# Optimization experiments

Measured on AMD Instinct MI355X. Metric: run time of the kernel, lower is better.

Reference implementation:

```python
import jax, jax.numpy as jnp
import numpy as np


def positional_encoding(n_tokens, d_model, dtype=jnp.float32):
    # standard sinusoidal PE: pe[pos, 2i] = sin(pos / 10000^(2i/d)), pe[pos, 2i+1] = cos(...)
    pos = jnp.arange(n_tokens, dtype=dtype)[:, None]            # [n, 1]
    i = jnp.arange(0, d_model, 2, dtype=dtype)[None, :]         # [1, d/2]
    angle = pos / jnp.power(jnp.asarray(10000.0, dtype), i / d_model)
    pe = jnp.zeros((n_tokens, d_model), dtype)
    pe = pe.at[:, 0::2].set(jnp.sin(angle))
    pe = pe.at[:, 1::2].set(jnp.cos(angle))
    return pe


def layer_norm(x, gamma, beta, eps=1e-5):
    mu = jnp.mean(x, axis=-1, keepdims=True)
    var = jnp.var(x, axis=-1, keepdims=True)
    return (x - mu) * jax.lax.rsqrt(var + eps) * gamma + beta


def setup_inputs() -> dict:
    key = jax.random.key(0)
    ks = jax.random.split(key, 4)
    b, n, d = 4, 1024, 1024
    dh = 1024  # dim_hidden_linear
    s = 1.0 / np.sqrt(d)
    return {
        "token_embedding": jax.random.normal(ks[0], (b, n, d), jnp.float32),
        "ln_gamma": jnp.ones((d,), jnp.float32),
        "ln_beta": jnp.zeros((d,), jnp.float32),
        "Wq": jax.random.normal(ks[1], (d, dh), jnp.float32) * s,
        "bq": jnp.zeros((dh,), jnp.float32),
        "Wk": jax.random.normal(ks[2], (d, dh), jnp.float32) * s,
        "bk": jnp.zeros((dh,), jnp.float32),
        "Wv": jax.random.normal(ks[3], (d, dh), jnp.float32) * s,
        "bv": jnp.zeros((dh,), jnp.float32),
        "num_heads": 16,
    }


def reference(token_embedding, ln_gamma, ln_beta, Wq, bq, Wk, bk, Wv, bv, num_heads):
    b, n, d = token_embedding.shape
    pe = positional_encoding(n, d)                      # [n, d]
    x = token_embedding + pe[None, :, :]                # broadcast over batch
    x = layer_norm(x, ln_gamma, ln_beta)
    q = x @ Wq + bq                                     # [b, n, dh]
    k = x @ Wk + bk
    v = x @ Wv + bv
    dh = q.shape[-1]
    hd = dh // num_heads                                # per-head dim
    q = q.reshape(b, n, num_heads, hd)
    k = k.reshape(b, n, num_heads, hd)
    v = v.reshape(b, n, num_heads, hd)
    scale = 1.0 / jnp.sqrt(jnp.asarray(hd, q.dtype))
    scores = jnp.einsum("bqhd,bkhd->bhqk", q, k) * scale  # [b, h, n, n]
    attn = jax.nn.softmax(scores, axis=-1)
    out = jnp.einsum("bhqk,bkhd->bqhd", attn, v)          # [b, n, h, hd]
    return out.reshape(b, n, dh)
```

## Files before the change

### kernel.cpp

```cpp
#include <hip/hip_runtime.h>
#include <hip/hip_bf16.h>
#include <math.h>

typedef __attribute__((ext_vector_type(8))) short bf16x8;
typedef __attribute__((ext_vector_type(4))) short bf16x4;
typedef __attribute__((ext_vector_type(4))) float f32x4;

static __device__ __forceinline__ void gld16(const void* g, void* l) {
    __builtin_amdgcn_global_load_lds(
        (const __attribute__((address_space(1))) unsigned int*)g,
        (__attribute__((address_space(3))) unsigned int*)l, 16, 0, 0);
}

static __device__ __forceinline__ short f2bf_s(float f) {
    __hip_bfloat16 h = __float2bfloat16(f);
    short s;
    __builtin_memcpy(&s, &h, 2);
    return s;
}

__global__ __launch_bounds__(256) void peln_wt_kernel(
    const float* __restrict__ emb,
    const float* __restrict__ gamma,
    const float* __restrict__ beta,
    const float* __restrict__ Wq,
    const float* __restrict__ Wk,
    const float* __restrict__ Wv,
    __hip_bfloat16* __restrict__ x,
    __hip_bfloat16* __restrict__ Wt)
{
    const int tid = threadIdx.x;
    if (blockIdx.x < 4096) {
        const int row = blockIdx.x;
        const int t   = row & 1023;
        float4 e = ((const float4*)(emb + (size_t)row * 1024))[tid];
        float v[4] = {e.x, e.y, e.z, e.w};
        float s = 0.f, ss = 0.f;
        #pragma unroll
        for (int kk = 0; kk < 4; ++kk) {
            int c = tid * 4 + kk;
            float ang = (float)t * exp2f(-13.287712379549449f * (float)(c >> 1) * (1.0f / 512.0f));
            float pe  = (c & 1) ? __cosf(ang) : __sinf(ang);
            v[kk] += pe;
            s  += v[kk];
            ss += v[kk] * v[kk];
        }
        #pragma unroll
        for (int off = 1; off < 64; off <<= 1) {
            s  += __shfl_xor(s, off);
            ss += __shfl_xor(ss, off);
        }
        __shared__ float red_s[4], red_ss[4];
        int wave = tid >> 6, lane = tid & 63;
        if (lane == 0) { red_s[wave] = s; red_ss[wave] = ss; }
        __syncthreads();
        float S  = red_s[0] + red_s[1] + red_s[2] + red_s[3];
        float SS = red_ss[0] + red_ss[1] + red_ss[2] + red_ss[3];
        float mu   = S * (1.0f / 1024.0f);
        float var  = SS * (1.0f / 1024.0f) - mu * mu;
        float rstd = rsqrtf(var + 1e-5f);
        #pragma unroll
        for (int kk = 0; kk < 4; ++kk) {
            int c = tid * 4 + kk;
            float y = (v[kk] - mu) * rstd * gamma[c] + beta[c];
            x[(size_t)row * 1024 + c] = __float2bfloat16(y);
        }
    } else {
        __shared__ __hip_bfloat16 tile[32][33];
        int wid = blockIdx.x - 4096;
        int zz  = wid >> 10;
        int rem = wid & 1023;
        int bx = rem & 31, by = rem >> 5;
        int tx = tid & 31, ty = tid >> 5;
        const float* src = (zz == 0) ? Wq : (zz == 1) ? Wk : Wv;
        __hip_bfloat16* dst = Wt + (size_t)zz * 1024 * 1024;
        int x0 = bx * 32, y0 = by * 32;
        #pragma unroll
        for (int kk = 0; kk < 4; ++kk)
            tile[ty + 8 * kk][tx] =
                __float2bfloat16(src[(size_t)(y0 + ty + 8 * kk) * 1024 + x0 + tx]);
        __syncthreads();
        #pragma unroll
        for (int kk = 0; kk < 4; ++kk)
            dst[(size_t)(x0 + ty + 8 * kk) * 1024 + y0 + tx] = tile[tx][ty + 8 * kk];
    }
}

__global__ __launch_bounds__(256) void qkv_gemm(
    const __hip_bfloat16* __restrict__ X,
    const __hip_bfloat16* __restrict__ Wt,
    const float* __restrict__ bq,
    const float* __restrict__ bk,
    const float* __restrict__ bv,
    __hip_bfloat16* __restrict__ qkv,
    __hip_bfloat16* __restrict__ vt)
{
    union SMem {
        struct { __hip_bfloat16 A[128 * 64]; __hip_bfloat16 B[128 * 64]; } s;
        __hip_bfloat16 C[128 * 132];
    };
    __shared__ __align__(16) SMem sm;

    const int id   = blockIdx.x;
    const int xcd  = id & 7;
    const int rest = id >> 3;
    const int j    = rest % 3;
    const int mblk = rest / 3;
    const int m0   = mblk * 128;
    const int n0   = (xcd * 3 + j) * 128;
    const int t    = n0 >> 10;
    const int nn0  = n0 & 1023;
    const __hip_bfloat16* W = Wt + (size_t)t * 1024 * 1024;

    const int tid  = threadIdx.x;
    const int wave = tid >> 6, lane = tid & 63;
    const int wm = wave & 1, wn = wave >> 1;
    const int lm = lane & 15, quad = lane >> 4;

    const int srow = lane >> 3;
    const int skc  = ((lane & 7) ^ srow) * 8;
    const int rbase = wave * 32;
    const __hip_bfloat16* gA = X + (size_t)(m0 + rbase + srow) * 1024 + skc;
    const __hip_bfloat16* gB = W + (size_t)(nn0 + rbase + srow) * 1024 + skc;
    __hip_bfloat16* lA = sm.s.A + rbase * 64;
    __hip_bfloat16* lB = sm.s.B + rbase * 64;

    f32x4 acc[4][4];
    #pragma unroll
    for (int i = 0; i < 4; ++i)
        #pragma unroll
        for (int jj = 0; jj < 4; ++jj)
            acc[i][jj] = (f32x4){0.f, 0.f, 0.f, 0.f};

    #pragma unroll
    for (int n = 0; n < 4; ++n) {
        gld16(gA + (size_t)n * 8 * 1024, lA + n * 8 * 64);
        gld16(gB + (size_t)n * 8 * 1024, lB + n * 8 * 64);
    }

    for (int k0 = 0; k0 < 1024; k0 += 64) {
        __syncthreads();

        bf16x8 a[2][4], b[2][4];
        #pragma unroll
        for (int ks = 0; ks < 2; ++ks) {
            #pragma unroll
            for (int i = 0; i < 4; ++i) {
                int row = wm * 64 + i * 16 + lm;
                a[ks][i] = *(const bf16x8*)(sm.s.A + (size_t)row * 64
                                            + (((ks * 4 + quad) ^ (lm & 7)) * 8));
            }
            #pragma unroll
            for (int jj = 0; jj < 4; ++jj) {
                int row = wn * 64 + jj * 16 + lm;
                b[ks][jj] = *(const bf16x8*)(sm.s.B + (size_t)row * 64
                                             + (((ks * 4 + quad) ^ (lm & 7)) * 8));
            }
        }
        __syncthreads();

        if (k0 + 64 < 1024) {
            #pragma unroll
            for (int n = 0; n < 4; ++n) {
                gld16(gA + (size_t)n * 8 * 1024 + k0 + 64, lA + n * 8 * 64);
                gld16(gB + (size_t)n * 8 * 1024 + k0 + 64, lB + n * 8 * 64);
            }
        }

        #pragma unroll
        for (int ks = 0; ks < 2; ++ks)
            #pragma unroll
            for (int i = 0; i < 4; ++i)
                #pragma unroll
                for (int jj = 0; jj < 4; ++jj)
                    acc[i][jj] = __builtin_amdgcn_mfma_f32_16x16x32_bf16(a[ks][i], b[ks][jj], acc[i][jj], 0, 0, 0);
    }

    const float* bias = (t == 0) ? bq : (t == 1) ? bk : bv;
    if (t < 2) {
        #pragma unroll
        for (int jj = 0; jj < 4; ++jj) {
            int col = wn * 64 + jj * 16 + lm;
            float bb = bias[nn0 + col];
            #pragma unroll
            for (int i = 0; i < 4; ++i)
                #pragma unroll
                for (int r = 0; r < 4; ++r) {
                    int row = wm * 64 + i * 16 + quad * 4 + r;
                    sm.C[(size_t)row * 132 + col] = __float2bfloat16(acc[i][jj][r] + bb);
                }
        }
        __syncthreads();
        __hip_bfloat16* out = qkv + (size_t)t * 4096 * 1024;
        #pragma unroll
        for (int c = 0; c < 8; ++c) {
            int g = tid + 256 * c;
            int row = g >> 4;
            int colc = (g & 15) * 8;
            bf16x8 vch = *(const bf16x8*)&sm.C[(size_t)row * 132 + colc];
            *(bf16x8*)(out + (size_t)(m0 + row) * 1024 + nn0 + colc) = vch;
        }
    } else {
        #pragma unroll
        for (int jj = 0; jj < 4; ++jj) {
            int col = wn * 64 + jj * 16 + lm;
            float bb = bias[nn0 + col];
            #pragma unroll
            for (int i = 0; i < 4; ++i)
                #pragma unroll
                for (int r = 0; r < 4; ++r) {
                    int row = wm * 64 + i * 16 + quad * 4 + r;
                    sm.C[(size_t)col * 132 + row] = __float2bfloat16(acc[i][jj][r] + bb);
                }
        }
        __syncthreads();
        const int bbase = (m0 >> 10) * 16 + (nn0 >> 6);
        const int mloc  = m0 & 1023;
        #pragma unroll
        for (int c = 0; c < 8; ++c) {
            int g = tid + 256 * c;
            int col = g >> 4;
            int rch = (g & 15) * 8;
            bf16x8 vch = *(const bf16x8*)&sm.C[(size_t)col * 132 + rch];
            int bh = bbase + (col >> 6);
            int d  = col & 63;
            *(bf16x8*)(vt + ((size_t)bh * 64 + d) * 1024 + mloc + rch) = vch;
        }
    }
}

__global__ __launch_bounds__(256, 2) void attn_kernel(
    const __hip_bfloat16* __restrict__ q,
    const __hip_bfloat16* __restrict__ k,
    const __hip_bfloat16* __restrict__ vt,
    float* __restrict__ out)
{
    __shared__ __align__(16) __hip_bfloat16 Kbuf[128 * 64];
    __shared__ __align__(16) __hip_bfloat16 Vbuf[2][64 * 64];
    __shared__ short ldsPT[4][32][72];
    const int id   = blockIdx.x;
    const int bh   = (id & 7) * 8 + ((id >> 3) & 7);
    const int qblk = id >> 6;
    const int b = bh >> 4, h = bh & 15;
    const int wave = threadIdx.x >> 6, lane = threadIdx.x & 63;
    const int lm = lane & 15, quad = lane >> 4;
    const int qbase = qblk * 128 + wave * 32;
    const float CEXP = 0.18033688011112042f;

    bf16x8 bqf[2][2];
    #pragma unroll
    for (int i = 0; i < 2; ++i)
        #pragma unroll
        for (int ks = 0; ks < 2; ++ks)
            bqf[i][ks] = *(const bf16x8*)(q + (size_t)(b * 1024 + qbase + 16 * i + lm) * 1024
                                            + h * 64 + ks * 32 + quad * 8);

    const __hip_bfloat16* kg = k + (size_t)(b * 1024) * 1024 + h * 64;
    const __hip_bfloat16* vg = vt + (size_t)bh * 64 * 1024;
    const int srow = lane >> 3;
    const int skc  = ((lane & 7) ^ srow) * 8;

    f32x4 OT[4][2];
    float li[2] = {0.f, 0.f};
    #pragma unroll
    for (int nt = 0; nt < 4; ++nt)
        #pragma unroll
        for (int i = 0; i < 2; ++i)
            OT[nt][i] = (f32x4){0.f, 0.f, 0.f, 0.f};

    for (int kt = 0; kt < 1024; kt += 128) {
        #pragma unroll
        for (int n = 0; n < 4; ++n) {
            int r0 = wave * 32 + n * 8;
            gld16(kg + (size_t)(kt + r0 + srow) * 1024 + skc, Kbuf + r0 * 64);
        }
        {
            int half = wave >> 1;
            #pragma unroll
            for (int n = 0; n < 4; ++n) {
                int d0 = (wave & 1) * 32 + n * 8;
                gld16(vg + (size_t)(d0 + srow) * 1024 + kt + half * 64 + skc,
                      Vbuf[half] + d0 * 64);
            }
        }
        __syncthreads();

        #pragma unroll
        for (int sr = 0; sr < 2; ++sr) {
            bf16x8 ak[4][2], av[4][2];
            #pragma unroll
            for (int jt = 0; jt < 4; ++jt)
                #pragma unroll
                for (int ks = 0; ks < 2; ++ks)
                    ak[jt][ks] = *(const bf16x8*)(Kbuf + (size_t)(sr * 64 + 16 * jt + lm) * 64
                                                  + (((ks * 4 + quad) ^ (lm & 7)) * 8));
            #pragma unroll
            for (int nt = 0; nt < 4; ++nt)
                #pragma unroll
                for (int ks = 0; ks < 2; ++ks)
                    av[nt][ks] = *(const bf16x8*)(Vbuf[sr] + (size_t)(16 * nt + lm) * 64
                                                  + (((ks * 4 + quad) ^ (lm & 7)) * 8));
            if (sr == 1) __syncthreads();

            f32x4 ST[2][4];
            #pragma unroll
            for (int i = 0; i < 2; ++i)
                #pragma unroll
                for (int jt = 0; jt < 4; ++jt)
                    ST[i][jt] = (f32x4){0.f, 0.f, 0.f, 0.f};
            #pragma unroll
            for (int ks = 0; ks < 2; ++ks)
                #pragma unroll
                for (int i = 0; i < 2; ++i)
                    #pragma unroll
                    for (int jt = 0; jt < 4; ++jt)
                        ST[i][jt] = __builtin_amdgcn_mfma_f32_16x16x32_bf16(ak[jt][ks], bqf[i][ks], ST[i][jt], 0, 0, 0);

            #pragma unroll
            for (int i = 0; i < 2; ++i)
                #pragma unroll
                for (int jt = 0; jt < 4; ++jt) {
                    bf16x4 pk;
                    #pragma unroll
                    for (int r = 0; r < 4; ++r) {
                        float p = __builtin_amdgcn_exp2f(ST[i][jt][r] * CEXP);
                        li[i] += p;
                        pk[r] = f2bf_s(p);
                    }
                    *(bf16x4*)&ldsPT[wave][16 * i + lm][16 * jt + quad * 4] = pk;
                }

            bf16x8 bp[2][2];
            #pragma unroll
            for (int i = 0; i < 2; ++i)
                #pragma unroll
                for (int ks = 0; ks < 2; ++ks)
                    bp[i][ks] = *(const bf16x8*)&ldsPT[wave][16 * i + lm][ks * 32 + quad * 8];
            #pragma unroll
            for (int ks = 0; ks < 2; ++ks)
                #pragma unroll
                for (int nt = 0; nt < 4; ++nt)
                    #pragma unroll
                    for (int i = 0; i < 2; ++i)
                        OT[nt][i] = __builtin_amdgcn_mfma_f32_16x16x32_bf16(av[nt][ks], bp[i][ks], OT[nt][i], 0, 0, 0);
        }
    }

    #pragma unroll
    for (int i = 0; i < 2; ++i) {
        li[i] += __shfl_xor(li[i], 16);
        li[i] += __shfl_xor(li[i], 32);
    }

    #pragma unroll
    for (int i = 0; i < 2; ++i) {
        float inv = 1.0f / li[i];
        int qrow = qbase + 16 * i + lm;
        #pragma unroll
        for (int nt = 0; nt < 4; ++nt) {
            float4 o4 = {OT[nt][i][0] * inv, OT[nt][i][1] * inv,
                         OT[nt][i][2] * inv, OT[nt][i][3] * inv};
            *(float4*)(out + (size_t)(b * 1024 + qrow) * 1024 + h * 64 + 16 * nt + quad * 4) = o4;
        }
    }
}

extern "C" void kernel_launch(void* const* d_in, const int* in_sizes, int n_in,
                              void* d_out, int out_size, void* d_ws, size_t ws_size,
                              hipStream_t stream)
{
    const float* emb   = (const float*)d_in[0];
    const float* gamma = (const float*)d_in[1];
    const float* beta  = (const float*)d_in[2];
    const float* Wq    = (const float*)d_in[3];
    const float* bq    = (const float*)d_in[4];
    const float* Wk    = (const float*)d_in[5];
    const float* bk    = (const float*)d_in[6];
    const float* Wv    = (const float*)d_in[7];
    const float* bv    = (const float*)d_in[8];
    float* out = (float*)d_out;

    __hip_bfloat16* ws  = (__hip_bfloat16*)d_ws;
    __hip_bfloat16* x   = ws;
    __hip_bfloat16* Wt  = x   + (size_t)4096 * 1024;
    __hip_bfloat16* qkv = Wt  + (size_t)3 * 1024 * 1024;
    __hip_bfloat16* vt  = qkv + (size_t)2 * 4096 * 1024;

    peln_wt_kernel<<<4096 + 3072, 256, 0, stream>>>(emb, gamma, beta, Wq, Wk, Wv, x, Wt);
    qkv_gemm<<<768, 256, 0, stream>>>(x, Wt, bq, bk, bv, qkv, vt);
    attn_kernel<<<512, 256, 0, stream>>>(qkv, qkv + (size_t)4096 * 1024, vt, out);
}
```

Measured before the change: 147.9 us.

## Rework QKV GEMM into 256x256 tiles with double-buffered quadrant-phased pipeline

```diff
diff --git a/kernel.cpp b/kernel.cpp
--- a/kernel.cpp
+++ b/kernel.cpp
@@ -86,7 +86,7 @@
     }
 }
 
-__global__ __launch_bounds__(256) void qkv_gemm(
+__global__ __launch_bounds__(512, 2) void qkv_gemm(
     const __hip_bfloat16* __restrict__ X,
     const __hip_bfloat16* __restrict__ Wt,
     const float* __restrict__ bq,
@@ -96,135 +96,161 @@
     __hip_bfloat16* __restrict__ vt)
 {
     union SMem {
-        struct { __hip_bfloat16 A[128 * 64]; __hip_bfloat16 B[128 * 64]; } s;
-        __hip_bfloat16 C[128 * 132];
+        struct { __hip_bfloat16 A[2][256 * 64]; __hip_bfloat16 B[2][256 * 64]; } s;
+        __hip_bfloat16 C[128 * 264];
     };
     __shared__ __align__(16) SMem sm;
 
     const int id   = blockIdx.x;
-    const int xcd  = id & 7;
-    const int rest = id >> 3;
-    const int j    = rest % 3;
-    const int mblk = rest / 3;
-    const int m0   = mblk * 128;
-    const int n0   = (xcd * 3 + j) * 128;
-    const int t    = n0 >> 10;
-    const int nn0  = n0 & 1023;
-    const __hip_bfloat16* W = Wt + (size_t)t * 1024 * 1024;
+    const int wgid = (id & 7) * 24 + (id >> 3);
+    const int mb   = wgid / 12;
+    const int nbt  = wgid % 12;
+    const int m0   = mb * 256;
+    const int t    = nbt >> 2;
+    const int nn0  = (nbt & 3) * 256;
 
     const int tid  = threadIdx.x;
-    const int wave = tid >> 6, lane = tid & 63;
-    const int wm = wave & 1, wn = wave >> 1;
+    const int w8   = tid >> 6;
+    const int lane = tid & 63;
+    const int wm = w8 & 1, wn = w8 >> 1;
     const int lm = lane & 15, quad = lane >> 4;
-
     const int srow = lane >> 3;
     const int skc  = ((lane & 7) ^ srow) * 8;
-    const int rbase = wave * 32;
-    const __hip_bfloat16* gA = X + (size_t)(m0 + rbase + srow) * 1024 + skc;
-    const __hip_bfloat16* gB = W + (size_t)(nn0 + rbase + srow) * 1024 + skc;
-    __hip_bfloat16* lA = sm.s.A + rbase * 64;
-    __hip_bfloat16* lB = sm.s.B + rbase * 64;
-
-    f32x4 acc[4][4];
+
+    const __hip_bfloat16* Ag = X  + (size_t)m0 * 1024;
+    const __hip_bfloat16* Bg = Wt + (size_t)t * 1024 * 1024 + (size_t)nn0 * 1024;
+
+    auto stA = [&](int buf, int h, int kt) {
+        __hip_bfloat16* l = &sm.s.A[buf][(h * 128 + w8 * 16) * 64];
+        const __hip_bfloat16* g = Ag + (size_t)(h * 128 + w8 * 16 + srow) * 1024 + kt + skc;
+        gld16(g, l);
+        gld16(g + (size_t)8 * 1024, l + 8 * 64);
+    };
+    auto stB = [&](int buf, int h, int kt) {
+        __hip_bfloat16* l = &sm.s.B[buf][(h * 128 + w8 * 16) * 64];
+        const __hip_bfloat16* g = Bg + (size_t)(h * 128 + w8 * 16 + srow) * 1024 + kt + skc;
+        gld16(g, l);
+        gld16(g + (size_t)8 * 1024, l + 8 * 64);
+    };
+
+    f32x4 acc[8][4];
     #pragma unroll
-    for (int i = 0; i < 4; ++i)
-        #pragma unroll
-        for (int jj = 0; jj < 4; ++jj)
-            acc[i][jj] = (f32x4){0.f, 0.f, 0.f, 0.f};
-
-    #pragma unroll
-    for (int n = 0; n < 4; ++n) {
-        gld16(gA + (size_t)n * 8 * 1024, lA + n * 8 * 64);
-        gld16(gB + (size_t)n * 8 * 1024, lB + n * 8 * 64);
-    }
-
-    for (int k0 = 0; k0 < 1024; k0 += 64) {
-        __syncthreads();
-
-        bf16x8 a[2][4], b[2][4];
-        #pragma unroll
-        for (int ks = 0; ks < 2; ++ks) {
-            #pragma unroll
-            for (int i = 0; i < 4; ++i) {
-                int row = wm * 64 + i * 16 + lm;
-                a[ks][i] = *(const bf16x8*)(sm.s.A + (size_t)row * 64
-                                            + (((ks * 4 + quad) ^ (lm & 7)) * 8));
+    for (int i = 0; i < 8; ++i)
+        #pragma unroll
+        for (int j = 0; j < 4; ++j)
+            acc[i][j] = (f32x4){0.f, 0.f, 0.f, 0.f};
+
+    stB(0, 0, 0);  stA(0, 0, 0);  stA(0, 1, 0);  stB(0, 1, 0);
+    stB(1, 0, 64); stA(1, 0, 64);
+    asm volatile("s_waitcnt vmcnt(4)" ::: "memory");
+    __builtin_amdgcn_s_barrier();
+
+#define QPHASE(MQ, NQ, STAGE, TAIL) do {                                        \
+    bf16x8 af[2][4], bb_[2][2];                                                 \
+    _Pragma("unroll")                                                           \
+    for (int ks = 0; ks < 2; ++ks) {                                            \
+        _Pragma("unroll")                                                       \
+        for (int mi = 0; mi < 4; ++mi)                                          \
+            af[ks][mi] = *(const bf16x8*)(Ab                                    \
+                + (size_t)((MQ) * 128 + wm * 64 + mi * 16 + lm) * 64            \
+                + (((ks * 4 + quad) ^ (lm & 7)) * 8));                          \
+        _Pragma("unroll")                                                       \
+        for (int ni = 0; ni < 2; ++ni)                                          \
+            bb_[ks][ni] = *(const bf16x8*)(Bb                                   \
+                + (size_t)((NQ) * 128 + wn * 32 + ni * 16 + lm) * 64            \
+                + (((ks * 4 + quad) ^ (lm & 7)) * 8));                          \
+    }                                                                           \
+    STAGE                                                                       \
+    __builtin_amdgcn_s_barrier();                                               \
+    asm volatile("s_waitcnt lgkmcnt(0)" ::: "memory");                          \
+    __builtin_amdgcn_sched_barrier(0);                                          \
+    __builtin_amdgcn_s_setprio(1);                                              \
+    _Pragma("unroll")                                                           \
+    for (int ks = 0; ks < 2; ++ks)                                              \
+        _Pragma("unroll")                                                       \
+        for (int mi = 0; mi < 4; ++mi)                                          \
+            _Pragma("unroll")                                                   \
+            for (int ni = 0; ni < 2; ++ni)                                      \
+                acc[(MQ) * 4 + mi][(NQ) * 2 + ni] =                             \
+                    __builtin_amdgcn_mfma_f32_16x16x32_bf16(af[ks][mi],         \
+                        bb_[ks][ni], acc[(MQ) * 4 + mi][(NQ) * 2 + ni], 0, 0, 0);\
+    __builtin_amdgcn_s_setprio(0);                                              \
+    TAIL                                                                        \
+    __builtin_amdgcn_s_barrier();                                               \
+} while (0)
+
+    for (int tt = 0; tt < 16; ++tt) {
+        const __hip_bfloat16* Ab = sm.s.A[tt & 1];
+        const __hip_bfloat16* Bb = sm.s.B[tt & 1];
+        QPHASE(0, 0, { if (tt + 1 < 16) stA((tt + 1) & 1, 1, (tt + 1) * 64); }, {});
+        QPHASE(1, 0, { if (tt + 1 < 16) stB((tt + 1) & 1, 1, (tt + 1) * 64); }, {});
+        QPHASE(0, 1, { if (tt + 2 < 16) stB(tt & 1, 0, (tt + 2) * 64); }, {});
+        QPHASE(1, 1, { if (tt + 2 < 16) stA(tt & 1, 0, (tt + 2) * 64); },
+               { if (tt < 14)       asm volatile("s_waitcnt vmcnt(4)" ::: "memory");
+                 else if (tt == 14) asm volatile("s_waitcnt vmcnt(0)" ::: "memory"); });
+    }
+#undef QPHASE
+
+    __syncthreads();
+
+    if (t < 2) {
+        const float* bias = (t == 0) ? bq : bk;
+        __hip_bfloat16* outp = qkv + (size_t)t * 4096 * 1024;
+        #pragma unroll
+        for (int H = 0; H < 2; ++H) {
+            if (H) __syncthreads();
+            #pragma unroll
+            for (int mi = 0; mi < 4; ++mi) {
+                int lrow = wm * 64 + mi * 16 + quad * 4;
+                #pragma unroll
+                for (int n = 0; n < 4; ++n) {
+                    int lcol = (n >> 1) * 128 + wn * 32 + (n & 1) * 16 + lm;
+                    float bb = bias[nn0 + lcol];
+                    #pragma unroll
+                    for (int r = 0; r < 4; ++r)
+                        sm.C[(size_t)(lrow + r) * 264 + lcol] =
+                            __float2bfloat16(acc[H * 4 + mi][n][r] + bb);
+                }
             }
-            #pragma unroll
-            for (int jj = 0; jj < 4; ++jj) {
-                int row = wn * 64 + jj * 16 + lm;
-                b[ks][jj] = *(const bf16x8*)(sm.s.B + (size_t)row * 64
-                                             + (((ks * 4 + quad) ^ (lm & 7)) * 8));
+            __syncthreads();
+            #pragma unroll
+            for (int c = 0; c < 8; ++c) {
+                int g   = tid + 512 * c;
+                int row = g >> 5;
+                int col = (g & 31) * 8;
+                bf16x8 vch = *(const bf16x8*)&sm.C[(size_t)row * 264 + col];
+                *(bf16x8*)(outp + (size_t)(m0 + H * 128 + row) * 1024 + nn0 + col) = vch;
             }
         }
-        __syncthreads();
-
-        if (k0 + 64 < 1024) {
-            #pragma unroll
-            for (int n = 0; n < 4; ++n) {
-                gld16(gA + (size_t)n * 8 * 1024 + k0 + 64, lA + n * 8 * 64);
-                gld16(gB + (size_t)n * 8 * 1024 + k0 + 64, lB + n * 8 * 64);
+    } else {
+        const int b0 = m0 >> 10, tok0 = m0 & 1023;
+        #pragma unroll
+        for (int H = 0; H < 2; ++H) {
+            if (H) __syncthreads();
+            #pragma unroll
+            for (int ni = 0; ni < 2; ++ni) {
+                int lcol = wn * 32 + ni * 16 + lm;
+                float bb = bv[nn0 + H * 128 + lcol];
+                #pragma unroll
+                for (int m = 0; m < 8; ++m) {
+                    int grow = (m >> 2) * 128 + wm * 64 + (m & 3) * 16 + quad * 4;
+                    #pragma unroll
+                    for (int r = 0; r < 4; ++r)
+                        sm.C[(size_t)lcol * 264 + grow + r] =
+                            __float2bfloat16(acc[m][H * 2 + ni][r] + bb);
+                }
             }
-        }
-
-        #pragma unroll
-        for (int ks = 0; ks < 2; ++ks)
-            #pragma unroll
-            for (int i = 0; i < 4; ++i)
-                #pragma unroll
-                for (int jj = 0; jj < 4; ++jj)
-                    acc[i][jj] = __builtin_amdgcn_mfma_f32_16x16x32_bf16(a[ks][i], b[ks][jj], acc[i][jj], 0, 0, 0);
-    }
-
-    const float* bias = (t == 0) ? bq : (t == 1) ? bk : bv;
-    if (t < 2) {
-        #pragma unroll
-        for (int jj = 0; jj < 4; ++jj) {
-            int col = wn * 64 + jj * 16 + lm;
-            float bb = bias[nn0 + col];
-            #pragma unroll
-            for (int i = 0; i < 4; ++i)
-                #pragma unroll
-                for (int r = 0; r < 4; ++r) {
-                    int row = wm * 64 + i * 16 + quad * 4 + r;
-                    sm.C[(size_t)row * 132 + col] = __float2bfloat16(acc[i][jj][r] + bb);
-                }
-        }
-        __syncthreads();
-        __hip_bfloat16* out = qkv + (size_t)t * 4096 * 1024;
-        #pragma unroll
-        for (int c = 0; c < 8; ++c) {
-            int g = tid + 256 * c;
-            int row = g >> 4;
-            int colc = (g & 15) * 8;
-            bf16x8 vch = *(const bf16x8*)&sm.C[(size_t)row * 132 + colc];
-            *(bf16x8*)(out + (size_t)(m0 + row) * 1024 + nn0 + colc) = vch;
-        }
-    } else {
-        #pragma unroll
-        for (int jj = 0; jj < 4; ++jj) {
-            int col = wn * 64 + jj * 16 + lm;
-            float bb = bias[nn0 + col];
-            #pragma unroll
-            for (int i = 0; i < 4; ++i)
-                #pragma unroll
-                for (int r = 0; r < 4; ++r) {
-                    int row = wm * 64 + i * 16 + quad * 4 + r;
-                    sm.C[(size_t)col * 132 + row] = __float2bfloat16(acc[i][jj][r] + bb);
-                }
-        }
-        __syncthreads();
-        const int bbase = (m0 >> 10) * 16 + (nn0 >> 6);
-        const int mloc  = m0 & 1023;
-        #pragma unroll
-        for (int c = 0; c < 8; ++c) {
-            int g = tid + 256 * c;
-            int col = g >> 4;
-            int rch = (g & 15) * 8;
-            bf16x8 vch = *(const bf16x8*)&sm.C[(size_t)col * 132 + rch];
-            int bh = bbase + (col >> 6);
-            int d  = col & 63;
-            *(bf16x8*)(vt + ((size_t)bh * 64 + d) * 1024 + mloc + rch) = vch;
+            __syncthreads();
+            #pragma unroll
+            for (int c = 0; c < 8; ++c) {
+                int g  = tid + 512 * c;
+                int d  = g >> 5;
+                int tc = (g & 31) * 8;
+                int dg = nn0 + H * 128 + d;
+                int bh = b0 * 16 + (dg >> 6);
+                bf16x8 vch = *(const bf16x8*)&sm.C[(size_t)d * 264 + tc];
+                *(bf16x8*)(vt + ((size_t)bh * 64 + (dg & 63)) * 1024 + tok0 + tc) = vch;
+            }
         }
     }
 }
@@ -387,6 +413,6 @@
     __hip_bfloat16* vt  = qkv + (size_t)2 * 4096 * 1024;
 
     peln_wt_kernel<<<4096 + 3072, 256, 0, stream>>>(emb, gamma, beta, Wq, Wk, Wv, x, Wt);
-    qkv_gemm<<<768, 256, 0, stream>>>(x, Wt, bq, bk, bv, qkv, vt);
+    qkv_gemm<<<192, 512, 0, stream>>>(x, Wt, bq, bk, bv, qkv, vt);
     attn_kernel<<<512, 256, 0, stream>>>(qkv, qkv + (size_t)4096 * 1024, vt, out);
 }
```

New measurement: 155.4 us. +5.1%, slower.

## Double-buffer K/V tiles in LDS and swizzle the P staging buffer

Applied to the files above, without the earlier changes.

```diff
diff --git a/kernel.cpp b/kernel.cpp
--- a/kernel.cpp
+++ b/kernel.cpp
@@ -235,9 +235,9 @@
     const __hip_bfloat16* __restrict__ vt,
     float* __restrict__ out)
 {
-    __shared__ __align__(16) __hip_bfloat16 Kbuf[128 * 64];
-    __shared__ __align__(16) __hip_bfloat16 Vbuf[2][64 * 64];
-    __shared__ short ldsPT[4][32][72];
+    __shared__ __align__(16) __hip_bfloat16 Kbuf[2][128 * 64];
+    __shared__ __align__(16) __hip_bfloat16 Vbuf[2][2][64 * 64];
+    __shared__ short ldsPT[4][32 * 64];
     const int id   = blockIdx.x;
     const int bh   = (id & 7) * 8 + ((id >> 3) & 7);
     const int qblk = id >> 6;
@@ -268,39 +268,45 @@
         for (int i = 0; i < 2; ++i)
             OT[nt][i] = (f32x4){0.f, 0.f, 0.f, 0.f};
 
-    for (int kt = 0; kt < 1024; kt += 128) {
+    auto stageKV = [&](int buf, int kt) {
         #pragma unroll
         for (int n = 0; n < 4; ++n) {
             int r0 = wave * 32 + n * 8;
-            gld16(kg + (size_t)(kt + r0 + srow) * 1024 + skc, Kbuf + r0 * 64);
-        }
-        {
-            int half = wave >> 1;
-            #pragma unroll
-            for (int n = 0; n < 4; ++n) {
-                int d0 = (wave & 1) * 32 + n * 8;
-                gld16(vg + (size_t)(d0 + srow) * 1024 + kt + half * 64 + skc,
-                      Vbuf[half] + d0 * 64);
-            }
-        }
-        __syncthreads();
+            gld16(kg + (size_t)(kt + r0 + srow) * 1024 + skc, Kbuf[buf] + r0 * 64);
+        }
+        int half = wave >> 1;
+        #pragma unroll
+        for (int n = 0; n < 4; ++n) {
+            int d0 = (wave & 1) * 32 + n * 8;
+            gld16(vg + (size_t)(d0 + srow) * 1024 + kt + half * 64 + skc,
+                  Vbuf[buf][half] + d0 * 64);
+        }
+    };
+
+    stageKV(0, 0);
+
+    for (int tt = 0; tt < 8; ++tt) {
+        __syncthreads();
+        if (tt + 1 < 8) stageKV((tt + 1) & 1, (tt + 1) * 128);
+
+        const __hip_bfloat16* Kb = Kbuf[tt & 1];
 
         #pragma unroll
         for (int sr = 0; sr < 2; ++sr) {
+            const __hip_bfloat16* Vb = Vbuf[tt & 1][sr];
             bf16x8 ak[4][2], av[4][2];
             #pragma unroll
             for (int jt = 0; jt < 4; ++jt)
                 #pragma unroll
                 for (int ks = 0; ks < 2; ++ks)
-                    ak[jt][ks] = *(const bf16x8*)(Kbuf + (size_t)(sr * 64 + 16 * jt + lm) * 64
+                    ak[jt][ks] = *(const bf16x8*)(Kb + (size_t)(sr * 64 + 16 * jt + lm) * 64
                                                   + (((ks * 4 + quad) ^ (lm & 7)) * 8));
             #pragma unroll
             for (int nt = 0; nt < 4; ++nt)
                 #pragma unroll
                 for (int ks = 0; ks < 2; ++ks)
-                    av[nt][ks] = *(const bf16x8*)(Vbuf[sr] + (size_t)(16 * nt + lm) * 64
+                    av[nt][ks] = *(const bf16x8*)(Vb + (size_t)(16 * nt + lm) * 64
                                                   + (((ks * 4 + quad) ^ (lm & 7)) * 8));
-            if (sr == 1) __syncthreads();
 
             f32x4 ST[2][4];
             #pragma unroll
@@ -327,7 +333,9 @@
                         li[i] += p;
                         pk[r] = f2bf_s(p);
                     }
-                    *(bf16x4*)&ldsPT[wave][16 * i + lm][16 * jt + quad * 4] = pk;
+                    int u = jt * 2 + (quad >> 1);
+                    *(bf16x4*)&ldsPT[wave][(16 * i + lm) * 64
+                        + ((u ^ (lm & 7)) << 3) + (quad & 1) * 4] = pk;
                 }
 
             bf16x8 bp[2][2];
@@ -335,7 +343,8 @@
             for (int i = 0; i < 2; ++i)
                 #pragma unroll
                 for (int ks = 0; ks < 2; ++ks)
-                    bp[i][ks] = *(const bf16x8*)&ldsPT[wave][16 * i + lm][ks * 32 + quad * 8];
+                    bp[i][ks] = *(const bf16x8*)&ldsPT[wave][(16 * i + lm) * 64
+                        + (((ks * 4 + quad) ^ (lm & 7)) << 3)];
             #pragma unroll
             for (int ks = 0; ks < 2; ++ks)
                 #pragma unroll
```

After: 149.9 us. No clear change (+1.3%).
